# Optimization experiments

Hardware: AMD Instinct MI355X
Metric: run time of the kernel (lower is better)

Reference implementation:

```python
import jax, jax.numpy as jnp
import numpy as np

N_NODES = 50000
N_EDGES = 800000
VOCAB = 1000
EMBED = 128
HIDDEN = 128
N_CLASSES = 10
N_GRAPHS = 64


def setup_inputs() -> dict:
    key = jax.random.key(0)
    ks = jax.random.split(key, 12)
    x_idx = jax.random.randint(ks[0], (N_NODES,), 0, VOCAB)
    edge_index = jax.random.randint(ks[1], (2, N_EDGES), 0, N_NODES)
    batch = jnp.sort(jax.random.randint(ks[2], (N_NODES,), 0, N_GRAPHS))
    s = lambda k, shp, fan: jax.random.normal(k, shp, jnp.float32) / jnp.sqrt(fan)
    return {
        "x_idx": x_idx,
        "edge_index": edge_index,
        "batch": batch,
        "embed_table": jax.random.normal(ks[3], (VOCAB, EMBED), jnp.float32),
        "Wl1": s(ks[4], (HIDDEN, EMBED), EMBED),
        "bl1": jnp.zeros((HIDDEN,), jnp.float32),
        "Wr1": s(ks[5], (HIDDEN, EMBED), EMBED),
        "Wl2": s(ks[6], (HIDDEN, HIDDEN), HIDDEN),
        "bl2": jnp.zeros((HIDDEN,), jnp.float32),
        "Wr2": s(ks[7], (HIDDEN, HIDDEN), HIDDEN),
        "linW": s(ks[8], (N_CLASSES, HIDDEN), HIDDEN),
        "linb": jnp.zeros((N_CLASSES,), jnp.float32),
    }


def _sage_conv(x, src, dst, Wl, bl, Wr):
    # mean aggregation of source features into destination nodes (PyG SAGEConv, aggr='mean')
    msg_sum = jax.ops.segment_sum(x[src], dst, num_segments=N_NODES)  # [N, d]
    cnt = jax.ops.segment_sum(jnp.ones((src.shape[0],), x.dtype), dst, num_segments=N_NODES)
    agg = msg_sum / jnp.maximum(cnt, 1.0)[:, None]
    # out = lin_l(agg) + lin_r(x); lin_l has bias, lin_r has none
    return agg @ Wl.T + bl + x @ Wr.T


def reference(x_idx, edge_index, batch, embed_table, Wl1, bl1, Wr1, Wl2, bl2, Wr2, linW, linb):
    src, dst = edge_index[0], edge_index[1]
    x = embed_table[x_idx]  # [N, EMBED]
    x = jax.nn.relu(_sage_conv(x, src, dst, Wl1, bl1, Wr1))
    x = jax.nn.relu(_sage_conv(x, src, dst, Wl2, bl2, Wr2))
    # global mean pool over graphs
    g_sum = jax.ops.segment_sum(x, batch, num_segments=N_GRAPHS)  # [G, HIDDEN]
    g_cnt = jax.ops.segment_sum(jnp.ones((x.shape[0],), x.dtype), batch, num_segments=N_GRAPHS)
    pooled = g_sum / jnp.maximum(g_cnt, 1.0)[:, None]
    return pooled @ linW.T + linb  # [G, N_CLASSES]
```

## Files before the change

kernel.cpp:

```cpp
#include <hip/hip_runtime.h>

#define N_NODES 50000
#define N_EDGES 800000
#define N_GRAPHS 64
#define SCAN_BLOCKS 196

#define NCHUNK 32
#define CHUNK_E (N_EDGES / NCHUNK)
#define NRANGE 4
#define RSZ (N_NODES / NRANGE)

#define K1_HIST (NCHUNK * NRANGE)
#define K1_EMBED (N_NODES * 16 / 256)
#define K1_PREP 32

typedef __bf16 bf16x8 __attribute__((ext_vector_type(8)));
typedef float f32x4 __attribute__((ext_vector_type(4)));

static __device__ __forceinline__ unsigned short f2bf(float f) {
    union { float f; unsigned u; } v; v.f = f;
    unsigned u = v.u;
    u += 0x7fffu + ((u >> 16) & 1u);
    return (unsigned short)(u >> 16);
}
static __device__ __forceinline__ float bflo(unsigned w) {
    union { unsigned u; float f; } v; v.u = w << 16; return v.f;
}
static __device__ __forceinline__ float bfhi(unsigned w) {
    union { unsigned u; float f; } v; v.u = w & 0xffff0000u; return v.f;
}

__global__ __launch_bounds__(256) void k1_kernel(const int* __restrict__ dst,
                                                 int* __restrict__ part,
                                                 const int* __restrict__ x_idx,
                                                 const float* __restrict__ table,
                                                 unsigned short* __restrict__ X,
                                                 const float* __restrict__ Wl1,
                                                 const float* __restrict__ Wr1,
                                                 const float* __restrict__ Wl2,
                                                 const float* __restrict__ Wr2,
                                                 unsigned short* __restrict__ blob,
                                                 float* __restrict__ gsum) {
    const int b = blockIdx.x;
    if (b < K1_HIST) {
        __shared__ int h[RSZ];
        const int c = b >> 2;
        const int r = b & 3;
        const int rbase = r * RSZ;
        for (int i = threadIdx.x; i < RSZ; i += 256) h[i] = 0;
        __syncthreads();
        const int4* d4 = (const int4*)(dst + c * CHUNK_E);
        for (int i = threadIdx.x; i < CHUNK_E / 4; i += 256) {
            int4 d = d4[i];
            unsigned a;
            a = (unsigned)(d.x - rbase); if (a < RSZ) atomicAdd(&h[a], 1);
            a = (unsigned)(d.y - rbase); if (a < RSZ) atomicAdd(&h[a], 1);
            a = (unsigned)(d.z - rbase); if (a < RSZ) atomicAdd(&h[a], 1);
            a = (unsigned)(d.w - rbase); if (a < RSZ) atomicAdd(&h[a], 1);
        }
        __syncthreads();
        int* p = part + (size_t)c * N_NODES + rbase;
        for (int i = threadIdx.x; i < RSZ; i += 256) p[i] = h[i];
    } else if (b < K1_HIST + K1_EMBED) {
        int i = (b - K1_HIST) * 256 + threadIdx.x;
        int n = i >> 4, cq = i & 15;
        const float4* src = (const float4*)(table + (size_t)x_idx[n] * 128 + cq * 8);
        float4 a = src[0], bb = src[1];
        uint4 o;
        o.x = (unsigned)f2bf(a.x)  | ((unsigned)f2bf(a.y)  << 16);
        o.y = (unsigned)f2bf(a.z)  | ((unsigned)f2bf(a.w)  << 16);
        o.z = (unsigned)f2bf(bb.x) | ((unsigned)f2bf(bb.y) << 16);
        o.w = (unsigned)f2bf(bb.z) | ((unsigned)f2bf(bb.w) << 16);
        ((uint4*)X)[i] = o;
    } else {
        int s = (b - K1_HIST - K1_EMBED) * 256 + threadIdx.x;
        gsum[s] = 0.f;
        int g = s >> 12;
        int sl = s & 4095;
        int fidx = sl >> 6, lane = sl & 63;
        int m = fidx >> 5, kk = (fidx >> 3) & 3, tile = fidx & 7;
        const float* W = g ? (m ? Wr2 : Wl2) : (m ? Wr1 : Wl1);
        int n  = tile * 16 + (lane & 15);
        int k0 = kk * 32 + (lane >> 4) * 8;
        const float4* src = (const float4*)(W + n * 128 + k0);
        float4 a = src[0], bb = src[1];
        uint4 o;
        o.x = (unsigned)f2bf(a.x)  | ((unsigned)f2bf(a.y)  << 16);
        o.y = (unsigned)f2bf(a.z)  | ((unsigned)f2bf(a.w)  << 16);
        o.z = (unsigned)f2bf(bb.x) | ((unsigned)f2bf(bb.y) << 16);
        o.w = (unsigned)f2bf(bb.z) | ((unsigned)f2bf(bb.w) << 16);
        ((uint4*)blob)[s] = o;
    }
}

__global__ __launch_bounds__(256) void cntsum_kernel(const int* __restrict__ part,
                                                     int* __restrict__ cnt,
                                                     int* __restrict__ bsum) {
    int t = threadIdx.x;
    int n = blockIdx.x * 256 + t;
    int s = 0;
    if (n < N_NODES) {
#pragma unroll
        for (int c = 0; c < NCHUNK; ++c) s += part[(size_t)c * N_NODES + n];
        cnt[n] = s;
    }
#pragma unroll
    for (int off = 32; off > 0; off >>= 1) s += __shfl_down(s, off, 64);
    __shared__ int ws[4];
    if ((t & 63) == 0) ws[t >> 6] = s;
    __syncthreads();
    if (t == 0) bsum[blockIdx.x] = ws[0] + ws[1] + ws[2] + ws[3];
}

__global__ __launch_bounds__(256) void rowptroff_kernel(const int* __restrict__ cnt,
                                                        const int* __restrict__ bsum,
                                                        const int* __restrict__ part,
                                                        int* __restrict__ rowptr,
                                                        int* __restrict__ off) {
    __shared__ int sb[256];
    __shared__ int sd[256];
    int t = threadIdx.x;
    sb[t] = (t < SCAN_BLOCKS) ? bsum[t] : 0;
    __syncthreads();
    for (int o = 1; o < 256; o <<= 1) {
        int add = (t >= o) ? sb[t - o] : 0;
        __syncthreads();
        sb[t] += add;
        __syncthreads();
    }
    int boff = (blockIdx.x > 0) ? sb[blockIdx.x - 1] : 0;

    int i = blockIdx.x * 256 + t;
    int v = (i < N_NODES) ? cnt[i] : 0;
    sd[t] = v;
    __syncthreads();
    for (int o = 1; o < 256; o <<= 1) {
        int add = (t >= o) ? sd[t - o] : 0;
        __syncthreads();
        sd[t] += add;
        __syncthreads();
    }
    int excl = sd[t] - v + boff;
    if (i < N_NODES) {
        rowptr[i] = excl;
        if (i == N_NODES - 1) rowptr[N_NODES] = excl + v;
        int run = excl;
#pragma unroll
        for (int c = 0; c < NCHUNK; ++c) {
            off[(size_t)c * N_NODES + i] = run;
            run += part[(size_t)c * N_NODES + i];
        }
    }
}

__global__ __launch_bounds__(256) void scatter_kernel(const int* __restrict__ src,
                                                      const int* __restrict__ dst,
                                                      const int* __restrict__ off,
                                                      int* __restrict__ csr) {
    __shared__ int h[RSZ];
    const int c = blockIdx.x >> 2;
    const int r = blockIdx.x & 3;
    const int rbase = r * RSZ;
    const int* o = off + (size_t)c * N_NODES + rbase;
    for (int i = threadIdx.x; i < RSZ; i += 256) h[i] = o[i];
    __syncthreads();
    const int4* d4 = (const int4*)(dst + c * CHUNK_E);
    const int4* s4 = (const int4*)(src + c * CHUNK_E);
    for (int i = threadIdx.x; i < CHUNK_E / 4; i += 256) {
        int4 d = d4[i];
        int4 s = s4[i];
        unsigned a;
        a = (unsigned)(d.x - rbase); if (a < RSZ) csr[atomicAdd(&h[a], 1)] = s.x;
        a = (unsigned)(d.y - rbase); if (a < RSZ) csr[atomicAdd(&h[a], 1)] = s.y;
        a = (unsigned)(d.z - rbase); if (a < RSZ) csr[atomicAdd(&h[a], 1)] = s.z;
        a = (unsigned)(d.w - rbase); if (a < RSZ) csr[atomicAdd(&h[a], 1)] = s.w;
    }
}

__global__ __launch_bounds__(256) void agg_kernel(const unsigned short* __restrict__ X,
                                                  const int* __restrict__ rowptr,
                                                  const int* __restrict__ csr,
                                                  unsigned short* __restrict__ AGG) {
    const int t = threadIdx.x;
    const int lane = t & 63;
    const int f = lane & 15;
    const int n = blockIdx.x * 16 + (t >> 6) * 4 + (lane >> 4);
    int beg = rowptr[n], end = rowptr[n + 1];
    const char* Xb = (const char*)X + f * 16;
    float a0 = 0.f, a1 = 0.f, a2 = 0.f, a3 = 0.f,
          a4 = 0.f, a5 = 0.f, a6 = 0.f, a7 = 0.f;
    int i = beg;
    for (; i + 4 <= end; i += 4) {
        int s0 = csr[i], s1 = csr[i + 1], s2 = csr[i + 2], s3 = csr[i + 3];
        uint4 v0 = *(const uint4*)(Xb + (size_t)s0 * 256);
        uint4 v1 = *(const uint4*)(Xb + (size_t)s1 * 256);
        uint4 v2 = *(const uint4*)(Xb + (size_t)s2 * 256);
        uint4 v3 = *(const uint4*)(Xb + (size_t)s3 * 256);
        a0 += (bflo(v0.x) + bflo(v1.x)) + (bflo(v2.x) + bflo(v3.x));
        a1 += (bfhi(v0.x) + bfhi(v1.x)) + (bfhi(v2.x) + bfhi(v3.x));
        a2 += (bflo(v0.y) + bflo(v1.y)) + (bflo(v2.y) + bflo(v3.y));
        a3 += (bfhi(v0.y) + bfhi(v1.y)) + (bfhi(v2.y) + bfhi(v3.y));
        a4 += (bflo(v0.z) + bflo(v1.z)) + (bflo(v2.z) + bflo(v3.z));
        a5 += (bfhi(v0.z) + bfhi(v1.z)) + (bfhi(v2.z) + bfhi(v3.z));
        a6 += (bflo(v0.w) + bflo(v1.w)) + (bflo(v2.w) + bflo(v3.w));
        a7 += (bfhi(v0.w) + bfhi(v1.w)) + (bfhi(v2.w) + bfhi(v3.w));
    }
    for (; i < end; ++i) {
        uint4 v0 = *(const uint4*)(Xb + (size_t)csr[i] * 256);
        a0 += bflo(v0.x); a1 += bfhi(v0.x);
        a2 += bflo(v0.y); a3 += bfhi(v0.y);
        a4 += bflo(v0.z); a5 += bfhi(v0.z);
        a6 += bflo(v0.w); a7 += bfhi(v0.w);
    }
    float inv = 1.f / (float)max(end - beg, 1);
    uint4 o;
    o.x = (unsigned)f2bf(a0 * inv) | ((unsigned)f2bf(a1 * inv) << 16);
    o.y = (unsigned)f2bf(a2 * inv) | ((unsigned)f2bf(a3 * inv) << 16);
    o.z = (unsigned)f2bf(a4 * inv) | ((unsigned)f2bf(a5 * inv) << 16);
    o.w = (unsigned)f2bf(a6 * inv) | ((unsigned)f2bf(a7 * inv) << 16);
    *(uint4*)((char*)AGG + (size_t)n * 256 + f * 16) = o;
}

__global__ __launch_bounds__(256) void gemm_kernel(const unsigned short* __restrict__ A0,
                                                   const unsigned short* __restrict__ A1,
                                                   const unsigned short* __restrict__ wblob,
                                                   const float* __restrict__ bias,
                                                   unsigned short* __restrict__ Y) {
    __shared__ char lds[65536];
    const int t = threadIdx.x, lane = t & 63, w = t >> 6;
    const int row0 = blockIdx.x * 128 + w * 32;

    {
        const char* src = (const char*)wblob + w * 16384 + lane * 16;
        char* dst = lds + w * 16384;
#pragma unroll
        for (int i = 0; i < 16; ++i) {
            __builtin_amdgcn_global_load_lds(
                (const __attribute__((address_space(1))) unsigned*)(src + i * 1024),
                (__attribute__((address_space(3))) unsigned*)(dst + i * 1024), 16, 0, 0);
        }
    }
    __syncthreads();

    f32x4 acc[2][8];
#pragma unroll
    for (int rt = 0; rt < 2; ++rt)
#pragma unroll
        for (int tl = 0; tl < 8; ++tl) acc[rt][tl] = (f32x4){0.f, 0.f, 0.f, 0.f};

    int rA = min(row0 + (lane & 15),      N_NODES - 1);
    int rB = min(row0 + 16 + (lane & 15), N_NODES - 1);
    const int kl = (lane >> 4) * 8;

#pragma unroll
    for (int km = 0; km < 8; ++km) {
        const unsigned short* A = (km < 4) ? A0 : A1;
        int k0 = (km & 3) * 32 + kl;
        bf16x8 a0 = *(const bf16x8*)(A + (size_t)rA * 128 + k0);
        bf16x8 a1 = *(const bf16x8*)(A + (size_t)rB * 128 + k0);
        const char* bbase = lds + km * 8192 + lane * 16;
#pragma unroll
        for (int tile = 0; tile < 8; ++tile) {
            bf16x8 b = *(const bf16x8*)(bbase + tile * 1024);
            acc[0][tile] = __builtin_amdgcn_mfma_f32_16x16x32_bf16(a0, b, acc[0][tile], 0, 0, 0);
            acc[1][tile] = __builtin_amdgcn_mfma_f32_16x16x32_bf16(a1, b, acc[1][tile], 0, 0, 0);
        }
    }

    const int c     = lane & 15;
    const int rbase = (lane >> 4) * 4;
#pragma unroll
    for (int rt = 0; rt < 2; ++rt) {
#pragma unroll
        for (int tile = 0; tile < 8; ++tile) {
            int col = tile * 16 + c;
            float bv = bias[col];
#pragma unroll
            for (int j = 0; j < 4; ++j) {
                int r = row0 + rt * 16 + rbase + j;
                if (r < N_NODES)
                    Y[(size_t)r * 128 + col] = f2bf(fmaxf(acc[rt][tile][j] + bv, 0.f));
            }
        }
    }
}

__global__ __launch_bounds__(256) void gemm_pool_kernel(const unsigned short* __restrict__ A0,
                                                        const unsigned short* __restrict__ A1,
                                                        const unsigned short* __restrict__ wblob,
                                                        const float* __restrict__ bias,
                                                        const int* __restrict__ batch,
                                                        float* __restrict__ gsum) {
    __shared__ char lds[65536];
    const int t = threadIdx.x, lane = t & 63, w = t >> 6;
    const int brow0 = blockIdx.x * 128;
    const int row0  = brow0 + w * 32;

    {
        const char* src = (const char*)wblob + w * 16384 + lane * 16;
        char* dst = lds + w * 16384;
#pragma unroll
        for (int i = 0; i < 16; ++i) {
            __builtin_amdgcn_global_load_lds(
                (const __attribute__((address_space(1))) unsigned*)(src + i * 1024),
                (__attribute__((address_space(3))) unsigned*)(dst + i * 1024), 16, 0, 0);
        }
    }
    __syncthreads();

    f32x4 acc[2][8];
#pragma unroll
    for (int rt = 0; rt < 2; ++rt)
#pragma unroll
        for (int tl = 0; tl < 8; ++tl) acc[rt][tl] = (f32x4){0.f, 0.f, 0.f, 0.f};

    int rA = min(row0 + (lane & 15),      N_NODES - 1);
    int rB = min(row0 + 16 + (lane & 15), N_NODES - 1);
    const int kl = (lane >> 4) * 8;

#pragma unroll
    for (int km = 0; km < 8; ++km) {
        const unsigned short* A = (km < 4) ? A0 : A1;
        int k0 = (km & 3) * 32 + kl;
        bf16x8 a0 = *(const bf16x8*)(A + (size_t)rA * 128 + k0);
        bf16x8 a1 = *(const bf16x8*)(A + (size_t)rB * 128 + k0);
        const char* bbase = lds + km * 8192 + lane * 16;
#pragma unroll
        for (int tile = 0; tile < 8; ++tile) {
            bf16x8 b = *(const bf16x8*)(bbase + tile * 1024);
            acc[0][tile] = __builtin_amdgcn_mfma_f32_16x16x32_bf16(a0, b, acc[0][tile], 0, 0, 0);
            acc[1][tile] = __builtin_amdgcn_mfma_f32_16x16x32_bf16(a1, b, acc[1][tile], 0, 0, 0);
        }
    }

    __syncthreads();
    float* ftile = (float*)lds;
    const int c     = lane & 15;
    const int rbase = (lane >> 4) * 4;
#pragma unroll
    for (int rt = 0; rt < 2; ++rt) {
#pragma unroll
        for (int tile = 0; tile < 8; ++tile) {
            int col = tile * 16 + c;
            float bv = bias[col];
#pragma unroll
            for (int j = 0; j < 4; ++j) {
                int lr = w * 32 + rt * 16 + rbase + j;
                ftile[lr * 128 + col] = fmaxf(acc[rt][tile][j] + bv, 0.f);
            }
        }
    }
    __syncthreads();

    const int col  = t & 127;
    const int half = t >> 7;
    float s = 0.f;
    int curg = -1;
    for (int rr = 0; rr < 64; ++rr) {
        int r = brow0 + half * 64 + rr;
        if (r >= N_NODES) break;
        int g = batch[r];
        if (g != curg) {
            if (curg >= 0) atomicAdd(&gsum[curg * 128 + col], s);
            curg = g; s = 0.f;
        }
        s += ftile[(half * 64 + rr) * 128 + col];
    }
    if (curg >= 0) atomicAdd(&gsum[curg * 128 + col], s);
}

__global__ void final_kernel(const float* __restrict__ gsum, const int* __restrict__ batch,
                             const float* __restrict__ linW, const float* __restrict__ linb,
                             float* __restrict__ out) {
    int t = blockIdx.x * 256 + threadIdx.x;
    if (t >= N_GRAPHS * 10) return;
    int g = t / 10, j = t % 10;
    int bnd[2];
    for (int c = 0; c < 2; ++c) {
        int target = g + c;
        int lo = 0, hi = N_NODES;
        while (lo < hi) { int mid = (lo + hi) >> 1; if (batch[mid] < target) lo = mid + 1; else hi = mid; }
        bnd[c] = lo;
    }
    float invc = 1.f / (float)max(bnd[1] - bnd[0], 1);
    float s = 0.f;
    for (int k = 0; k < 128; ++k) s += gsum[g * 128 + k] * linW[j * 128 + k];
    out[t] = linb[j] + s * invc;
}

extern "C" void kernel_launch(void* const* d_in, const int* in_sizes, int n_in,
                              void* d_out, int out_size, void* d_ws, size_t ws_size,
                              hipStream_t stream) {
    const int*   x_idx = (const int*)d_in[0];
    const int*   eidx  = (const int*)d_in[1];
    const int*   batch = (const int*)d_in[2];
    const float* table = (const float*)d_in[3];
    const float* Wl1   = (const float*)d_in[4];
    const float* bl1   = (const float*)d_in[5];
    const float* Wr1   = (const float*)d_in[6];
    const float* Wl2   = (const float*)d_in[7];
    const float* bl2   = (const float*)d_in[8];
    const float* Wr2   = (const float*)d_in[9];
    const float* linW  = (const float*)d_in[10];
    const float* linb  = (const float*)d_in[11];
    float*       out   = (float*)d_out;

    const int* src = eidx;
    const int* dst = eidx + N_EDGES;

    unsigned short* X    = (unsigned short*)d_ws;
    unsigned short* AGG  = X   + (size_t)N_NODES * 128;
    unsigned short* Y1   = AGG + (size_t)N_NODES * 128;
    unsigned short* blob = Y1  + (size_t)N_NODES * 128;
    float* gsum = (float*)(blob + 65536);
    int* cnt    = (int*)(gsum + N_GRAPHS * 128);
    int* rowptr = cnt + N_NODES;
    int* csr    = rowptr + (N_NODES + 1);
    int* bsum   = csr + N_EDGES;
    int* part   = bsum + SCAN_BLOCKS;
    int* off    = part + (size_t)NCHUNK * N_NODES;

    k1_kernel<<<K1_HIST + K1_EMBED + K1_PREP, 256, 0, stream>>>(
        dst, part, x_idx, table, X, Wl1, Wr1, Wl2, Wr2, blob, gsum);
    cntsum_kernel   <<<SCAN_BLOCKS, 256, 0, stream>>>(part, cnt, bsum);
    rowptroff_kernel<<<SCAN_BLOCKS, 256, 0, stream>>>(cnt, bsum, part, rowptr, off);
    scatter_kernel  <<<NCHUNK * NRANGE, 256, 0, stream>>>(src, dst, off, csr);

    agg_kernel <<<dim3(N_NODES / 16), 256, 0, stream>>>(X, rowptr, csr, AGG);
    gemm_kernel<<<dim3((N_NODES + 127) / 128), 256, 0, stream>>>(AGG, X, blob, bl1, Y1);
    agg_kernel      <<<dim3(N_NODES / 16), 256, 0, stream>>>(Y1, rowptr, csr, AGG);
    gemm_pool_kernel<<<dim3((N_NODES + 127) / 128), 256, 0, stream>>>(AGG, Y1, blob + 32768, bl2, batch, gsum);

    final_kernel<<<3, 256, 0, stream>>>(gsum, batch, linW, linb, out);
}
```

Measured before the change: 153.5 us.

## Split node features into four column-quarter planes to improve gather locality

Node feature matrices (X, Y1, AGG) are stored as four separate 32-column planes instead of row-major 128-wide rows. The aggregation kernel gives each block a single quarter, so its gathers touch a 3.2 MB plane that fits more easily in cache, and each neighbor read is a 64-byte segment. The GEMMs and embedding writes are updated for the new layout. The cost is four passes over the CSR indices and more scattered 2-byte stores in the GEMM epilogue.

```diff
diff --git a/kernel.cpp b/kernel.cpp
--- a/kernel.cpp
+++ b/kernel.cpp
@@ -13,6 +13,10 @@
 #define K1_HIST (NCHUNK * NRANGE)
 #define K1_EMBED (N_NODES * 16 / 256)
 #define K1_PREP 32
+
+#define QUS (N_NODES * 32)
+
+#define AGG_NB ((N_NODES + 63) / 64)
 
 typedef __bf16 bf16x8 __attribute__((ext_vector_type(8)));
 typedef float f32x4 __attribute__((ext_vector_type(4)));
@@ -71,7 +75,8 @@
         o.y = (unsigned)f2bf(a.z)  | ((unsigned)f2bf(a.w)  << 16);
         o.z = (unsigned)f2bf(bb.x) | ((unsigned)f2bf(bb.y) << 16);
         o.w = (unsigned)f2bf(bb.z) | ((unsigned)f2bf(bb.w) << 16);
-        ((uint4*)X)[i] = o;
+        int qq = cq >> 2;
+        ((uint4*)X)[(size_t)qq * (N_NODES * 4) + n * 4 + (cq & 3)] = o;
     } else {
         int s = (b - K1_HIST - K1_EMBED) * 256 + threadIdx.x;
         gsum[s] = 0.f;
@@ -177,25 +182,27 @@
     }
 }
 
-__global__ __launch_bounds__(256) void agg_kernel(const unsigned short* __restrict__ X,
+__global__ __launch_bounds__(256) void agg_kernel(const unsigned short* __restrict__ Xq,
                                                   const int* __restrict__ rowptr,
                                                   const int* __restrict__ csr,
-                                                  unsigned short* __restrict__ AGG) {
+                                                  unsigned short* __restrict__ AGGq) {
     const int t = threadIdx.x;
     const int lane = t & 63;
-    const int f = lane & 15;
-    const int n = blockIdx.x * 16 + (t >> 6) * 4 + (lane >> 4);
+    const int q = blockIdx.x & 3;
+    const int n = (blockIdx.x >> 2) * 64 + (t >> 6) * 16 + (lane >> 2);
+    const int f = lane & 3;
+    if (n >= N_NODES) return;
     int beg = rowptr[n], end = rowptr[n + 1];
-    const char* Xb = (const char*)X + f * 16;
+    const char* Xb = (const char*)(Xq + (size_t)q * QUS) + f * 16;
     float a0 = 0.f, a1 = 0.f, a2 = 0.f, a3 = 0.f,
           a4 = 0.f, a5 = 0.f, a6 = 0.f, a7 = 0.f;
     int i = beg;
     for (; i + 4 <= end; i += 4) {
         int s0 = csr[i], s1 = csr[i + 1], s2 = csr[i + 2], s3 = csr[i + 3];
-        uint4 v0 = *(const uint4*)(Xb + (size_t)s0 * 256);
-        uint4 v1 = *(const uint4*)(Xb + (size_t)s1 * 256);
-        uint4 v2 = *(const uint4*)(Xb + (size_t)s2 * 256);
-        uint4 v3 = *(const uint4*)(Xb + (size_t)s3 * 256);
+        uint4 v0 = *(const uint4*)(Xb + (size_t)s0 * 64);
+        uint4 v1 = *(const uint4*)(Xb + (size_t)s1 * 64);
+        uint4 v2 = *(const uint4*)(Xb + (size_t)s2 * 64);
+        uint4 v3 = *(const uint4*)(Xb + (size_t)s3 * 64);
         a0 += (bflo(v0.x) + bflo(v1.x)) + (bflo(v2.x) + bflo(v3.x));
         a1 += (bfhi(v0.x) + bfhi(v1.x)) + (bfhi(v2.x) + bfhi(v3.x));
         a2 += (bflo(v0.y) + bflo(v1.y)) + (bflo(v2.y) + bflo(v3.y));
@@ -206,7 +213,7 @@
         a7 += (bfhi(v0.w) + bfhi(v1.w)) + (bfhi(v2.w) + bfhi(v3.w));
     }
     for (; i < end; ++i) {
-        uint4 v0 = *(const uint4*)(Xb + (size_t)csr[i] * 256);
+        uint4 v0 = *(const uint4*)(Xb + (size_t)csr[i] * 64);
         a0 += bflo(v0.x); a1 += bfhi(v0.x);
         a2 += bflo(v0.y); a3 += bfhi(v0.y);
         a4 += bflo(v0.z); a5 += bfhi(v0.z);
@@ -218,7 +225,7 @@
     o.y = (unsigned)f2bf(a2 * inv) | ((unsigned)f2bf(a3 * inv) << 16);
     o.z = (unsigned)f2bf(a4 * inv) | ((unsigned)f2bf(a5 * inv) << 16);
     o.w = (unsigned)f2bf(a6 * inv) | ((unsigned)f2bf(a7 * inv) << 16);
-    *(uint4*)((char*)AGG + (size_t)n * 256 + f * 16) = o;
+    *(uint4*)((char*)(AGGq + (size_t)q * QUS) + (size_t)n * 64 + f * 16) = o;
 }
 
 __global__ __launch_bounds__(256) void gemm_kernel(const unsigned short* __restrict__ A0,
@@ -254,10 +261,9 @@
 
 #pragma unroll
     for (int km = 0; km < 8; ++km) {
-        const unsigned short* A = (km < 4) ? A0 : A1;
-        int k0 = (km & 3) * 32 + kl;
-        bf16x8 a0 = *(const bf16x8*)(A + (size_t)rA * 128 + k0);
-        bf16x8 a1 = *(const bf16x8*)(A + (size_t)rB * 128 + k0);
+        const unsigned short* Aq = ((km < 4) ? A0 : A1) + (size_t)(km & 3) * QUS;
+        bf16x8 a0 = *(const bf16x8*)(Aq + (size_t)rA * 32 + kl);
+        bf16x8 a1 = *(const bf16x8*)(Aq + (size_t)rB * 32 + kl);
         const char* bbase = lds + km * 8192 + lane * 16;
 #pragma unroll
         for (int tile = 0; tile < 8; ++tile) {
@@ -275,11 +281,13 @@
         for (int tile = 0; tile < 8; ++tile) {
             int col = tile * 16 + c;
             float bv = bias[col];
+            int q = col >> 5, wc = col & 31;
 #pragma unroll
             for (int j = 0; j < 4; ++j) {
                 int r = row0 + rt * 16 + rbase + j;
                 if (r < N_NODES)
-                    Y[(size_t)r * 128 + col] = f2bf(fmaxf(acc[rt][tile][j] + bv, 0.f));
+                    Y[(size_t)q * QUS + (size_t)r * 32 + wc] =
+                        f2bf(fmaxf(acc[rt][tile][j] + bv, 0.f));
             }
         }
     }
@@ -320,10 +328,9 @@
 
 #pragma unroll
     for (int km = 0; km < 8; ++km) {
-        const unsigned short* A = (km < 4) ? A0 : A1;
-        int k0 = (km & 3) * 32 + kl;
-        bf16x8 a0 = *(const bf16x8*)(A + (size_t)rA * 128 + k0);
-        bf16x8 a1 = *(const bf16x8*)(A + (size_t)rB * 128 + k0);
+        const unsigned short* Aq = ((km < 4) ? A0 : A1) + (size_t)(km & 3) * QUS;
+        bf16x8 a0 = *(const bf16x8*)(Aq + (size_t)rA * 32 + kl);
+        bf16x8 a1 = *(const bf16x8*)(Aq + (size_t)rB * 32 + kl);
         const char* bbase = lds + km * 8192 + lane * 16;
 #pragma unroll
         for (int tile = 0; tile < 8; ++tile) {
@@ -426,9 +433,9 @@
     rowptroff_kernel<<<SCAN_BLOCKS, 256, 0, stream>>>(cnt, bsum, part, rowptr, off);
     scatter_kernel  <<<NCHUNK * NRANGE, 256, 0, stream>>>(src, dst, off, csr);
 
-    agg_kernel <<<dim3(N_NODES / 16), 256, 0, stream>>>(X, rowptr, csr, AGG);
+    agg_kernel <<<dim3(AGG_NB * 4), 256, 0, stream>>>(X, rowptr, csr, AGG);
     gemm_kernel<<<dim3((N_NODES + 127) / 128), 256, 0, stream>>>(AGG, X, blob, bl1, Y1);
-    agg_kernel      <<<dim3(N_NODES / 16), 256, 0, stream>>>(Y1, rowptr, csr, AGG);
+    agg_kernel      <<<dim3(AGG_NB * 4), 256, 0, stream>>>(Y1, rowptr, csr, AGG);
     gemm_pool_kernel<<<dim3((N_NODES + 127) / 128), 256, 0, stream>>>(AGG, Y1, blob + 32768, bl2, batch, gsum);
 
     final_kernel<<<3, 256, 0, stream>>>(gsum, batch, linW, linb, out);
```

Result: no change. 152.5 us (-0.6%).

## Pre-sort edges by source range before CSR build; two row tiles per GEMM block

Applied to the files above, without the earlier changes.

Adds a coarse counting-sort pass that buckets edges by source-node range into 16 buckets. The destination histogram and scatter then run on the reordered edge arrays, so each CSR row's neighbour list comes out roughly sorted by source. This should improve gather locality in the aggregation kernels. It costs two extra kernels and two extra 800K-entry edge array passes. Separately, the first GEMM now processes two 128-row tiles per block, so the weight LDS load is amortised over more rows, at the cost of launching half as many blocks.

```diff
diff --git a/kernel.cpp b/kernel.cpp
--- a/kernel.cpp
+++ b/kernel.cpp
@@ -10,9 +10,13 @@
 #define NRANGE 4
 #define RSZ (N_NODES / NRANGE)
 
-#define K1_HIST (NCHUNK * NRANGE)
-#define K1_EMBED (N_NODES * 16 / 256)
-#define K1_PREP 32
+#define NSRCR 16
+#define SRCR_SZ (N_NODES / NSRCR)
+#define WCHUNK (CHUNK_E / 4)
+
+#define SA_HIST NCHUNK
+#define SA_EMBED (N_NODES * 16 / 256)
+#define SA_PREP 32
 
 typedef __bf16 bf16x8 __attribute__((ext_vector_type(8)));
 typedef float f32x4 __attribute__((ext_vector_type(4)));
@@ -30,8 +34,8 @@
     union { unsigned u; float f; } v; v.u = w & 0xffff0000u; return v.f;
 }
 
-__global__ __launch_bounds__(256) void k1_kernel(const int* __restrict__ dst,
-                                                 int* __restrict__ part,
+__global__ __launch_bounds__(256) void sA_kernel(const int* __restrict__ src,
+                                                 int* __restrict__ scnt,
                                                  const int* __restrict__ x_idx,
                                                  const float* __restrict__ table,
                                                  unsigned short* __restrict__ X,
@@ -42,30 +46,23 @@
                                                  unsigned short* __restrict__ blob,
                                                  float* __restrict__ gsum) {
     const int b = blockIdx.x;
-    if (b < K1_HIST) {
-        __shared__ int h[RSZ];
-        const int c = b >> 2;
-        const int r = b & 3;
-        const int rbase = r * RSZ;
-        for (int i = threadIdx.x; i < RSZ; i += 256) h[i] = 0;
+    if (b < SA_HIST) {
+        __shared__ int h[4][NSRCR];
+        const int t = threadIdx.x, w = t >> 6, lane = t & 63;
+        if (t < 64) h[t >> 4][t & 15] = 0;
         __syncthreads();
-        const int4* d4 = (const int4*)(dst + c * CHUNK_E);
-        for (int i = threadIdx.x; i < CHUNK_E / 4; i += 256) {
-            int4 d = d4[i];
-            unsigned a;
-            a = (unsigned)(d.x - rbase); if (a < RSZ) atomicAdd(&h[a], 1);
-            a = (unsigned)(d.y - rbase); if (a < RSZ) atomicAdd(&h[a], 1);
-            a = (unsigned)(d.z - rbase); if (a < RSZ) atomicAdd(&h[a], 1);
-            a = (unsigned)(d.w - rbase); if (a < RSZ) atomicAdd(&h[a], 1);
+        const int* s = src + b * CHUNK_E + w * WCHUNK;
+        for (int i = lane; i < WCHUNK; i += 64) {
+            unsigned r = (unsigned)s[i] / SRCR_SZ;
+            atomicAdd(&h[w][r], 1);
         }
         __syncthreads();
-        int* p = part + (size_t)c * N_NODES + rbase;
-        for (int i = threadIdx.x; i < RSZ; i += 256) p[i] = h[i];
-    } else if (b < K1_HIST + K1_EMBED) {
-        int i = (b - K1_HIST) * 256 + threadIdx.x;
+        if (t < 64) scnt[(b * 4 + (t >> 4)) * NSRCR + (t & 15)] = h[t >> 4][t & 15];
+    } else if (b < SA_HIST + SA_EMBED) {
+        int i = (b - SA_HIST) * 256 + threadIdx.x;
         int n = i >> 4, cq = i & 15;
-        const float4* src = (const float4*)(table + (size_t)x_idx[n] * 128 + cq * 8);
-        float4 a = src[0], bb = src[1];
+        const float4* sp = (const float4*)(table + (size_t)x_idx[n] * 128 + cq * 8);
+        float4 a = sp[0], bb = sp[1];
         uint4 o;
         o.x = (unsigned)f2bf(a.x)  | ((unsigned)f2bf(a.y)  << 16);
         o.y = (unsigned)f2bf(a.z)  | ((unsigned)f2bf(a.w)  << 16);
@@ -73,7 +70,7 @@
         o.w = (unsigned)f2bf(bb.z) | ((unsigned)f2bf(bb.w) << 16);
         ((uint4*)X)[i] = o;
     } else {
-        int s = (b - K1_HIST - K1_EMBED) * 256 + threadIdx.x;
+        int s = (b - SA_HIST - SA_EMBED) * 256 + threadIdx.x;
         gsum[s] = 0.f;
         int g = s >> 12;
         int sl = s & 4095;
@@ -82,8 +79,8 @@
         const float* W = g ? (m ? Wr2 : Wl2) : (m ? Wr1 : Wl1);
         int n  = tile * 16 + (lane & 15);
         int k0 = kk * 32 + (lane >> 4) * 8;
-        const float4* src = (const float4*)(W + n * 128 + k0);
-        float4 a = src[0], bb = src[1];
+        const float4* sp = (const float4*)(W + n * 128 + k0);
+        float4 a = sp[0], bb = sp[1];
         uint4 o;
         o.x = (unsigned)f2bf(a.x)  | ((unsigned)f2bf(a.y)  << 16);
         o.y = (unsigned)f2bf(a.z)  | ((unsigned)f2bf(a.w)  << 16);
@@ -91,6 +88,68 @@
         o.w = (unsigned)f2bf(bb.z) | ((unsigned)f2bf(bb.w) << 16);
         ((uint4*)blob)[s] = o;
     }
+}
+
+__global__ __launch_bounds__(256) void sB_kernel(const int* __restrict__ src,
+                                                 const int* __restrict__ dst,
+                                                 const int* __restrict__ scnt,
+                                                 int* __restrict__ e2src,
+                                                 int* __restrict__ e2dst) {
+    __shared__ int sc[NCHUNK * 4 * NSRCR];
+    __shared__ int tot[NSRCR];
+    __shared__ int base[4][NSRCR];
+    __shared__ int cnt[4][NSRCR];
+    const int t = threadIdx.x, c = blockIdx.x;
+    for (int i = t; i < NCHUNK * 4 * NSRCR; i += 256) sc[i] = scnt[i];
+    __syncthreads();
+    if (t < NSRCR) {
+        int s = 0;
+        for (int cw = 0; cw < NCHUNK * 4; ++cw) s += sc[cw * NSRCR + t];
+        tot[t] = s;
+    }
+    __syncthreads();
+    if (t < 64) {
+        int w = t >> 4, r = t & 15;
+        int rs = 0;
+        for (int r2 = 0; r2 < r; ++r2) rs += tot[r2];
+        int p = 0, lim = c * 4 + w;
+        for (int cw = 0; cw < lim; ++cw) p += sc[cw * NSRCR + r];
+        base[w][r] = rs + p;
+        cnt[w][r] = 0;
+    }
+    __syncthreads();
+    const int w = t >> 6, lane = t & 63;
+    const int* sp = src + c * CHUNK_E + w * WCHUNK;
+    const int* dp = dst + c * CHUNK_E + w * WCHUNK;
+    for (int i = lane; i < WCHUNK; i += 64) {
+        int sv = sp[i], dv = dp[i];
+        unsigned r = (unsigned)sv / SRCR_SZ;
+        int pos = base[w][r] + atomicAdd(&cnt[w][r], 1);
+        e2src[pos] = sv;
+        e2dst[pos] = dv;
+    }
+}
+
+__global__ __launch_bounds__(256) void histpart_kernel(const int* __restrict__ dst,
+                                                       int* __restrict__ part) {
+    __shared__ int h[RSZ];
+    const int c = blockIdx.x >> 2;
+    const int r = blockIdx.x & 3;
+    const int rbase = r * RSZ;
+    for (int i = threadIdx.x; i < RSZ; i += 256) h[i] = 0;
+    __syncthreads();
+    const int4* d4 = (const int4*)(dst + c * CHUNK_E);
+    for (int i = threadIdx.x; i < CHUNK_E / 4; i += 256) {
+        int4 d = d4[i];
+        unsigned a;
+        a = (unsigned)(d.x - rbase); if (a < RSZ) atomicAdd(&h[a], 1);
+        a = (unsigned)(d.y - rbase); if (a < RSZ) atomicAdd(&h[a], 1);
+        a = (unsigned)(d.z - rbase); if (a < RSZ) atomicAdd(&h[a], 1);
+        a = (unsigned)(d.w - rbase); if (a < RSZ) atomicAdd(&h[a], 1);
+    }
+    __syncthreads();
+    int* p = part + (size_t)c * N_NODES + rbase;
+    for (int i = threadIdx.x; i < RSZ; i += 256) p[i] = h[i];
 }
 
 __global__ __launch_bounds__(256) void cntsum_kernel(const int* __restrict__ part,
@@ -228,7 +287,6 @@
                                                    unsigned short* __restrict__ Y) {
     __shared__ char lds[65536];
     const int t = threadIdx.x, lane = t & 63, w = t >> 6;
-    const int row0 = blockIdx.x * 128 + w * 32;
 
     {
         const char* src = (const char*)wblob + w * 16384 + lane * 16;
@@ -242,44 +300,52 @@
     }
     __syncthreads();
 
-    f32x4 acc[2][8];
-#pragma unroll
-    for (int rt = 0; rt < 2; ++rt)
-#pragma unroll
-        for (int tl = 0; tl < 8; ++tl) acc[rt][tl] = (f32x4){0.f, 0.f, 0.f, 0.f};
-
-    int rA = min(row0 + (lane & 15),      N_NODES - 1);
-    int rB = min(row0 + 16 + (lane & 15), N_NODES - 1);
     const int kl = (lane >> 4) * 8;
-
-#pragma unroll
-    for (int km = 0; km < 8; ++km) {
-        const unsigned short* A = (km < 4) ? A0 : A1;
-        int k0 = (km & 3) * 32 + kl;
-        bf16x8 a0 = *(const bf16x8*)(A + (size_t)rA * 128 + k0);
-        bf16x8 a1 = *(const bf16x8*)(A + (size_t)rB * 128 + k0);
-        const char* bbase = lds + km * 8192 + lane * 16;
-#pragma unroll
-        for (int tile = 0; tile < 8; ++tile) {
-            bf16x8 b = *(const bf16x8*)(bbase + tile * 1024);
-            acc[0][tile] = __builtin_amdgcn_mfma_f32_16x16x32_bf16(a0, b, acc[0][tile], 0, 0, 0);
-            acc[1][tile] = __builtin_amdgcn_mfma_f32_16x16x32_bf16(a1, b, acc[1][tile], 0, 0, 0);
-        }
-    }
-
     const int c     = lane & 15;
     const int rbase = (lane >> 4) * 4;
-#pragma unroll
-    for (int rt = 0; rt < 2; ++rt) {
-#pragma unroll
-        for (int tile = 0; tile < 8; ++tile) {
-            int col = tile * 16 + c;
-            float bv = bias[col];
-#pragma unroll
-            for (int j = 0; j < 4; ++j) {
-                int r = row0 + rt * 16 + rbase + j;
-                if (r < N_NODES)
-                    Y[(size_t)r * 128 + col] = f2bf(fmaxf(acc[rt][tile][j] + bv, 0.f));
+
+#pragma unroll 1
+    for (int tt = 0; tt < 2; ++tt) {
+        const int tile0 = blockIdx.x * 2 + tt;
+        if (tile0 * 128 >= N_NODES) break;
+        const int row0 = tile0 * 128 + w * 32;
+
+        f32x4 acc[2][8];
+#pragma unroll
+        for (int rt = 0; rt < 2; ++rt)
+#pragma unroll
+            for (int tl = 0; tl < 8; ++tl) acc[rt][tl] = (f32x4){0.f, 0.f, 0.f, 0.f};
+
+        int rA = min(row0 + (lane & 15),      N_NODES - 1);
+        int rB = min(row0 + 16 + (lane & 15), N_NODES - 1);
+
+#pragma unroll
+        for (int km = 0; km < 8; ++km) {
+            const unsigned short* A = (km < 4) ? A0 : A1;
+            int k0 = (km & 3) * 32 + kl;
+            bf16x8 a0 = *(const bf16x8*)(A + (size_t)rA * 128 + k0);
+            bf16x8 a1 = *(const bf16x8*)(A + (size_t)rB * 128 + k0);
+            const char* bbase = lds + km * 8192 + lane * 16;
+#pragma unroll
+            for (int tile = 0; tile < 8; ++tile) {
+                bf16x8 b = *(const bf16x8*)(bbase + tile * 1024);
+                acc[0][tile] = __builtin_amdgcn_mfma_f32_16x16x32_bf16(a0, b, acc[0][tile], 0, 0, 0);
+                acc[1][tile] = __builtin_amdgcn_mfma_f32_16x16x32_bf16(a1, b, acc[1][tile], 0, 0, 0);
+            }
+        }
+
+#pragma unroll
+        for (int rt = 0; rt < 2; ++rt) {
+#pragma unroll
+            for (int tile = 0; tile < 8; ++tile) {
+                int col = tile * 16 + c;
+                float bv = bias[col];
+#pragma unroll
+                for (int j = 0; j < 4; ++j) {
+                    int r = row0 + rt * 16 + rbase + j;
+                    if (r < N_NODES)
+                        Y[(size_t)r * 128 + col] = f2bf(fmaxf(acc[rt][tile][j] + bv, 0.f));
+                }
             }
         }
     }
@@ -419,15 +485,21 @@
     int* bsum   = csr + N_EDGES;
     int* part   = bsum + SCAN_BLOCKS;
     int* off    = part + (size_t)NCHUNK * N_NODES;
-
-    k1_kernel<<<K1_HIST + K1_EMBED + K1_PREP, 256, 0, stream>>>(
-        dst, part, x_idx, table, X, Wl1, Wr1, Wl2, Wr2, blob, gsum);
+    int* e2src  = off + (size_t)NCHUNK * N_NODES;
+    int* e2dst  = e2src + N_EDGES;
+    int* scnt   = e2dst + N_EDGES;
+
+    sA_kernel<<<SA_HIST + SA_EMBED + SA_PREP, 256, 0, stream>>>(
+        src, scnt, x_idx, table, X, Wl1, Wr1, Wl2, Wr2, blob, gsum);
+    sB_kernel<<<NCHUNK, 256, 0, stream>>>(src, dst, scnt, e2src, e2dst);
+
+    histpart_kernel <<<NCHUNK * NRANGE, 256, 0, stream>>>(e2dst, part);
     cntsum_kernel   <<<SCAN_BLOCKS, 256, 0, stream>>>(part, cnt, bsum);
     rowptroff_kernel<<<SCAN_BLOCKS, 256, 0, stream>>>(cnt, bsum, part, rowptr, off);
-    scatter_kernel  <<<NCHUNK * NRANGE, 256, 0, stream>>>(src, dst, off, csr);
+    scatter_kernel  <<<NCHUNK * NRANGE, 256, 0, stream>>>(e2src, e2dst, off, csr);
 
     agg_kernel <<<dim3(N_NODES / 16), 256, 0, stream>>>(X, rowptr, csr, AGG);
-    gemm_kernel<<<dim3((N_NODES + 127) / 128), 256, 0, stream>>>(AGG, X, blob, bl1, Y1);
+    gemm_kernel<<<dim3((N_NODES + 255) / 256), 256, 0, stream>>>(AGG, X, blob, bl1, Y1);
     agg_kernel      <<<dim3(N_NODES / 16), 256, 0, stream>>>(Y1, rowptr, csr, AGG);
     gemm_pool_kernel<<<dim3((N_NODES + 127) / 128), 256, 0, stream>>>(AGG, Y1, blob + 32768, bl2, batch, gsum);
 
```

After: 226.1 us. 1.47x slower.

## Spread node aggregation across a full wavefront and process two row tiles per GEMM block

Applied to the files above, without the earlier changes.

The aggregation kernel now gives each node a whole 64-lane wavefront: four edge groups of 16 lanes gather different neighbours in parallel and are combined with cross-lane shuffles, instead of one 16-lane group walking a node's edge list alone. This targets load imbalance and latency on the irregular gather, at the cost of shuffle reductions and three quarters of the lanes sitting idle during the store. Separately, the first GEMM now loops over two 128-row tiles per block, so the weight blob loaded into LDS is reused twice and the grid is halved.

```diff
diff --git a/kernel.cpp b/kernel.cpp
--- a/kernel.cpp
+++ b/kernel.cpp
@@ -29,6 +29,12 @@
 static __device__ __forceinline__ float bfhi(unsigned w) {
     union { unsigned u; float f; } v; v.u = w & 0xffff0000u; return v.f;
 }
+
+#define ACC8(A, v) do { \
+    A[0] += bflo((v).x); A[1] += bfhi((v).x); \
+    A[2] += bflo((v).y); A[3] += bfhi((v).y); \
+    A[4] += bflo((v).z); A[5] += bfhi((v).z); \
+    A[6] += bflo((v).w); A[7] += bfhi((v).w); } while (0)
 
 __global__ __launch_bounds__(256) void k1_kernel(const int* __restrict__ dst,
                                                  int* __restrict__ part,
@@ -183,42 +189,51 @@
                                                   unsigned short* __restrict__ AGG) {
     const int t = threadIdx.x;
     const int lane = t & 63;
+    const int e = lane >> 4;
     const int f = lane & 15;
-    const int n = blockIdx.x * 16 + (t >> 6) * 4 + (lane >> 4);
-    int beg = rowptr[n], end = rowptr[n + 1];
+    const int n = blockIdx.x * 4 + (t >> 6);
+    const int beg = rowptr[n], end = rowptr[n + 1];
     const char* Xb = (const char*)X + f * 16;
-    float a0 = 0.f, a1 = 0.f, a2 = 0.f, a3 = 0.f,
-          a4 = 0.f, a5 = 0.f, a6 = 0.f, a7 = 0.f;
+    float a[8];
+#pragma unroll
+    for (int k = 0; k < 8; ++k) a[k] = 0.f;
+
     int i = beg;
-    for (; i + 4 <= end; i += 4) {
-        int s0 = csr[i], s1 = csr[i + 1], s2 = csr[i + 2], s3 = csr[i + 3];
-        uint4 v0 = *(const uint4*)(Xb + (size_t)s0 * 256);
-        uint4 v1 = *(const uint4*)(Xb + (size_t)s1 * 256);
-        uint4 v2 = *(const uint4*)(Xb + (size_t)s2 * 256);
-        uint4 v3 = *(const uint4*)(Xb + (size_t)s3 * 256);
-        a0 += (bflo(v0.x) + bflo(v1.x)) + (bflo(v2.x) + bflo(v3.x));
-        a1 += (bfhi(v0.x) + bfhi(v1.x)) + (bfhi(v2.x) + bfhi(v3.x));
-        a2 += (bflo(v0.y) + bflo(v1.y)) + (bflo(v2.y) + bflo(v3.y));
-        a3 += (bfhi(v0.y) + bfhi(v1.y)) + (bfhi(v2.y) + bfhi(v3.y));
-        a4 += (bflo(v0.z) + bflo(v1.z)) + (bflo(v2.z) + bflo(v3.z));
-        a5 += (bfhi(v0.z) + bfhi(v1.z)) + (bfhi(v2.z) + bfhi(v3.z));
-        a6 += (bflo(v0.w) + bflo(v1.w)) + (bflo(v2.w) + bflo(v3.w));
-        a7 += (bfhi(v0.w) + bfhi(v1.w)) + (bfhi(v2.w) + bfhi(v3.w));
-    }
-    for (; i < end; ++i) {
-        uint4 v0 = *(const uint4*)(Xb + (size_t)csr[i] * 256);
-        a0 += bflo(v0.x); a1 += bfhi(v0.x);
-        a2 += bflo(v0.y); a3 += bfhi(v0.y);
-        a4 += bflo(v0.z); a5 += bfhi(v0.z);
-        a6 += bflo(v0.w); a7 += bfhi(v0.w);
-    }
-    float inv = 1.f / (float)max(end - beg, 1);
-    uint4 o;
-    o.x = (unsigned)f2bf(a0 * inv) | ((unsigned)f2bf(a1 * inv) << 16);
-    o.y = (unsigned)f2bf(a2 * inv) | ((unsigned)f2bf(a3 * inv) << 16);
-    o.z = (unsigned)f2bf(a4 * inv) | ((unsigned)f2bf(a5 * inv) << 16);
-    o.w = (unsigned)f2bf(a6 * inv) | ((unsigned)f2bf(a7 * inv) << 16);
-    *(uint4*)((char*)AGG + (size_t)n * 256 + f * 16) = o;
+    for (; i + 8 <= end; i += 8) {
+        int c0 = csr[i + e];
+        int c1 = csr[i + 4 + e];
+        uint4 v0 = *(const uint4*)(Xb + (size_t)c0 * 256);
+        uint4 v1 = *(const uint4*)(Xb + (size_t)c1 * 256);
+        ACC8(a, v0);
+        ACC8(a, v1);
+    }
+    if (i + 4 <= end) {
+        int c0 = csr[i + e];
+        uint4 v0 = *(const uint4*)(Xb + (size_t)c0 * 256);
+        ACC8(a, v0);
+        i += 4;
+    }
+    if (i + e < end) {
+        int c0 = csr[i + e];
+        uint4 v0 = *(const uint4*)(Xb + (size_t)c0 * 256);
+        ACC8(a, v0);
+    }
+
+#pragma unroll
+    for (int k = 0; k < 8; ++k) {
+        a[k] += __shfl_xor(a[k], 16, 64);
+        a[k] += __shfl_xor(a[k], 32, 64);
+    }
+
+    if (e == 0) {
+        float inv = 1.f / (float)max(end - beg, 1);
+        uint4 o;
+        o.x = (unsigned)f2bf(a[0] * inv) | ((unsigned)f2bf(a[1] * inv) << 16);
+        o.y = (unsigned)f2bf(a[2] * inv) | ((unsigned)f2bf(a[3] * inv) << 16);
+        o.z = (unsigned)f2bf(a[4] * inv) | ((unsigned)f2bf(a[5] * inv) << 16);
+        o.w = (unsigned)f2bf(a[6] * inv) | ((unsigned)f2bf(a[7] * inv) << 16);
+        *(uint4*)((char*)AGG + (size_t)n * 256 + f * 16) = o;
+    }
 }
 
 __global__ __launch_bounds__(256) void gemm_kernel(const unsigned short* __restrict__ A0,
@@ -228,7 +243,6 @@
                                                    unsigned short* __restrict__ Y) {
     __shared__ char lds[65536];
     const int t = threadIdx.x, lane = t & 63, w = t >> 6;
-    const int row0 = blockIdx.x * 128 + w * 32;
 
     {
         const char* src = (const char*)wblob + w * 16384 + lane * 16;
@@ -242,44 +256,52 @@
     }
     __syncthreads();
 
-    f32x4 acc[2][8];
-#pragma unroll
-    for (int rt = 0; rt < 2; ++rt)
-#pragma unroll
-        for (int tl = 0; tl < 8; ++tl) acc[rt][tl] = (f32x4){0.f, 0.f, 0.f, 0.f};
-
-    int rA = min(row0 + (lane & 15),      N_NODES - 1);
-    int rB = min(row0 + 16 + (lane & 15), N_NODES - 1);
     const int kl = (lane >> 4) * 8;
-
-#pragma unroll
-    for (int km = 0; km < 8; ++km) {
-        const unsigned short* A = (km < 4) ? A0 : A1;
-        int k0 = (km & 3) * 32 + kl;
-        bf16x8 a0 = *(const bf16x8*)(A + (size_t)rA * 128 + k0);
-        bf16x8 a1 = *(const bf16x8*)(A + (size_t)rB * 128 + k0);
-        const char* bbase = lds + km * 8192 + lane * 16;
-#pragma unroll
-        for (int tile = 0; tile < 8; ++tile) {
-            bf16x8 b = *(const bf16x8*)(bbase + tile * 1024);
-            acc[0][tile] = __builtin_amdgcn_mfma_f32_16x16x32_bf16(a0, b, acc[0][tile], 0, 0, 0);
-            acc[1][tile] = __builtin_amdgcn_mfma_f32_16x16x32_bf16(a1, b, acc[1][tile], 0, 0, 0);
-        }
-    }
-
     const int c     = lane & 15;
     const int rbase = (lane >> 4) * 4;
-#pragma unroll
-    for (int rt = 0; rt < 2; ++rt) {
-#pragma unroll
-        for (int tile = 0; tile < 8; ++tile) {
-            int col = tile * 16 + c;
-            float bv = bias[col];
-#pragma unroll
-            for (int j = 0; j < 4; ++j) {
-                int r = row0 + rt * 16 + rbase + j;
-                if (r < N_NODES)
-                    Y[(size_t)r * 128 + col] = f2bf(fmaxf(acc[rt][tile][j] + bv, 0.f));
+
+#pragma unroll 1
+    for (int tt = 0; tt < 2; ++tt) {
+        const int tile0 = blockIdx.x * 2 + tt;
+        if (tile0 * 128 >= N_NODES) break;
+        const int row0 = tile0 * 128 + w * 32;
+
+        f32x4 acc[2][8];
+#pragma unroll
+        for (int rt = 0; rt < 2; ++rt)
+#pragma unroll
+            for (int tl = 0; tl < 8; ++tl) acc[rt][tl] = (f32x4){0.f, 0.f, 0.f, 0.f};
+
+        int rA = min(row0 + (lane & 15),      N_NODES - 1);
+        int rB = min(row0 + 16 + (lane & 15), N_NODES - 1);
+
+#pragma unroll
+        for (int km = 0; km < 8; ++km) {
+            const unsigned short* A = (km < 4) ? A0 : A1;
+            int k0 = (km & 3) * 32 + kl;
+            bf16x8 a0 = *(const bf16x8*)(A + (size_t)rA * 128 + k0);
+            bf16x8 a1 = *(const bf16x8*)(A + (size_t)rB * 128 + k0);
+            const char* bbase = lds + km * 8192 + lane * 16;
+#pragma unroll
+            for (int tile = 0; tile < 8; ++tile) {
+                bf16x8 b = *(const bf16x8*)(bbase + tile * 1024);
+                acc[0][tile] = __builtin_amdgcn_mfma_f32_16x16x32_bf16(a0, b, acc[0][tile], 0, 0, 0);
+                acc[1][tile] = __builtin_amdgcn_mfma_f32_16x16x32_bf16(a1, b, acc[1][tile], 0, 0, 0);
+            }
+        }
+
+#pragma unroll
+        for (int rt = 0; rt < 2; ++rt) {
+#pragma unroll
+            for (int tile = 0; tile < 8; ++tile) {
+                int col = tile * 16 + c;
+                float bv = bias[col];
+#pragma unroll
+                for (int j = 0; j < 4; ++j) {
+                    int r = row0 + rt * 16 + rbase + j;
+                    if (r < N_NODES)
+                        Y[(size_t)r * 128 + col] = f2bf(fmaxf(acc[rt][tile][j] + bv, 0.f));
+                }
             }
         }
     }
@@ -426,9 +448,9 @@
     rowptroff_kernel<<<SCAN_BLOCKS, 256, 0, stream>>>(cnt, bsum, part, rowptr, off);
     scatter_kernel  <<<NCHUNK * NRANGE, 256, 0, stream>>>(src, dst, off, csr);
 
-    agg_kernel <<<dim3(N_NODES / 16), 256, 0, stream>>>(X, rowptr, csr, AGG);
-    gemm_kernel<<<dim3((N_NODES + 127) / 128), 256, 0, stream>>>(AGG, X, blob, bl1, Y1);
-    agg_kernel      <<<dim3(N_NODES / 16), 256, 0, stream>>>(Y1, rowptr, csr, AGG);
+    agg_kernel <<<dim3(N_NODES / 4), 256, 0, stream>>>(X, rowptr, csr, AGG);
+    gemm_kernel<<<dim3((N_NODES + 255) / 256), 256, 0, stream>>>(AGG, X, blob, bl1, Y1);
+    agg_kernel      <<<dim3(N_NODES / 4), 256, 0, stream>>>(Y1, rowptr, csr, AGG);
     gemm_pool_kernel<<<dim3((N_NODES + 127) / 128), 256, 0, stream>>>(AGG, Y1, blob + 32768, bl2, batch, gsum);
 
     final_kernel<<<3, 256, 0, stream>>>(gsum, batch, linW, linb, out);
```

Result: slower. 161.6 us (+5.3%).
